# Kernel optimization log

Hardware: AMD Instinct MI355X
Metric: run time of the kernel (lower is better)

## Reference

```python
import jax, jax.numpy as jnp
import numpy as np

N_USER = 50000
N_ITEM = 50000
E = 600000
IN_F = 128
HID = 256
OUT = 256
HEADS = 4
D = HID // HEADS
EPS = 1e-5


def setup_inputs() -> dict:
    key = jax.random.key(0)
    ks = jax.random.split(key, 32)
    inp = {}
    inp['x_user'] = jax.random.normal(ks[0], (N_USER, IN_F), jnp.float32)
    inp['x_item'] = jax.random.normal(ks[1], (N_ITEM, IN_F), jnp.float32)
    inp['ui_src'] = jax.random.randint(ks[2], (E,), 0, N_USER)
    inp['ui_dst'] = jax.random.randint(ks[3], (E,), 0, N_ITEM)
    inp['iu_src'] = jax.random.randint(ks[4], (E,), 0, N_ITEM)
    inp['iu_dst'] = jax.random.randint(ks[5], (E,), 0, N_USER)
    dims = [IN_F, HID, HID, HID]
    i = 6
    for l in range(4):
        din = dims[l]
        inp['W%d' % (l + 1)] = jax.random.normal(ks[i], (2, din, HID), jnp.float32) * (1.0 / np.sqrt(din)); i += 1
        inp['al%d' % (l + 1)] = jax.random.normal(ks[i], (2, HEADS, D), jnp.float32) * 0.1; i += 1
        inp['ar%d' % (l + 1)] = jax.random.normal(ks[i], (2, HEADS, D), jnp.float32) * 0.1; i += 1
        inp['b%d' % (l + 1)] = jnp.zeros((2, HID), jnp.float32); i += 1
    inp['bn_g'] = jnp.ones((3, 2, HID), jnp.float32)
    inp['bn_b'] = jnp.zeros((3, 2, HID), jnp.float32)
    return inp


def gat_conv(x_src, x_dst, src, dst, W, al, ar, b, n_dst):
    # DGL GATConv: shared fc, per-head additive attention, segment softmax over dst.
    H, Dh = al.shape
    z_src = (x_src @ W).reshape(-1, H, Dh)   # [Ns,H,D]
    z_dst = (x_dst @ W).reshape(-1, H, Dh)   # [Nd,H,D]
    el = jnp.sum(z_src * al, axis=-1)        # [Ns,H]
    er = jnp.sum(z_dst * ar, axis=-1)        # [Nd,H]
    e = jax.nn.leaky_relu(el[src] + er[dst], 0.2)          # [E,H]
    m = jax.ops.segment_max(e, dst, num_segments=n_dst)    # [Nd,H]
    ex = jnp.exp(e - m[dst])
    s = jax.ops.segment_sum(ex, dst, num_segments=n_dst)
    alpha = ex / s[dst]                                    # [E,H]
    out = jax.ops.segment_sum(z_src[src] * alpha[:, :, None], dst, num_segments=n_dst)
    return out.reshape(n_dst, H * Dh) + b


def batchnorm(x, g, beta):
    mu = jnp.mean(x, axis=0)
    var = jnp.mean((x - mu) ** 2, axis=0)
    return (x - mu) * jax.lax.rsqrt(var + EPS) * g + beta


def _forward(x_user, x_item, ui_src, ui_dst, iu_src, iu_dst,
             W1, al1, ar1, b1, W2, al2, ar2, b2, W3, al3, ar3, b3, W4, al4, ar4, b4,
             bn_g, bn_b):
    def layer(hu, hi, W, al, ar, b):
        h_item = gat_conv(hu, hi, ui_src, ui_dst, W[0], al[0], ar[0], b[0], N_ITEM)
        h_user = gat_conv(hi, hu, iu_src, iu_dst, W[1], al[1], ar[1], b[1], N_USER)
        return h_user, h_item  # mean over single relation per dst type = identity

    hu, hi = layer(x_user, x_item, W1, al1, ar1, b1)
    hu = jax.nn.leaky_relu(batchnorm(hu, bn_g[0, 0], bn_b[0, 0]), 0.01)
    hi = jax.nn.leaky_relu(batchnorm(hi, bn_g[0, 1], bn_b[0, 1]), 0.01)
    hu, hi = layer(hu, hi, W2, al2, ar2, b2)
    hu = jax.nn.leaky_relu(batchnorm(hu, bn_g[1, 0], bn_b[1, 0]), 0.01)
    hi = jax.nn.leaky_relu(batchnorm(hi, bn_g[1, 1], bn_b[1, 1]), 0.01)
    hu, hi = layer(hu, hi, W3, al3, ar3, b3)
    hu = jnp.tanh(batchnorm(hu, bn_g[2, 0], bn_b[2, 0]))
    hi = jnp.tanh(batchnorm(hi, bn_g[2, 1], bn_b[2, 1]))
    hu, hi = layer(hu, hi, W4, al4, ar4, b4)
    return hu.reshape(-1, OUT), hi.reshape(-1, OUT)


def reference(x_user, x_item, ui_src, ui_dst, iu_src, iu_dst,
              W1, al1, ar1, b1, W2, al2, ar2, b2, W3, al3, ar3, b3, W4, al4, ar4, b4,
              bn_g, bn_b):
    return _forward(x_user, x_item, ui_src, ui_dst, iu_src, iu_dst,
                    W1, al1, ar1, b1, W2, al2, ar2, b2, W3, al3, ar3, b3,
                    W4, al4, ar4, b4, bn_g, bn_b)
```

## Files before the change

### kernel.cpp

```cpp
#include <hip/hip_runtime.h>
#include <hip/hip_bf16.h>
#include <type_traits>

#define NN 50000
#define NE 600000
#define HF 256

typedef float f32x4 __attribute__((ext_vector_type(4)));
typedef _Float16 f16x8 __attribute__((ext_vector_type(8)));
typedef _Float16 f16x4 __attribute__((ext_vector_type(4)));

__global__ __launch_bounds__(256) void k_tofp16_2(const float* __restrict__ A,
                                                  const float* __restrict__ B,
                                                  _Float16* __restrict__ OA,
                                                  _Float16* __restrict__ OB, int n4) {
  int i = blockIdx.x * 256 + threadIdx.x;
  const float* X = (i < n4) ? A : B;
  _Float16* Y = (i < n4) ? OA : OB;
  int j = (i < n4) ? i : i - n4;
  if (j < n4) {
    float4 v = reinterpret_cast<const float4*>(X)[j];
    f16x4 o = {(_Float16)v.x, (_Float16)v.y, (_Float16)v.z, (_Float16)v.w};
    reinterpret_cast<f16x4*>(Y)[j] = o;
  }
}

struct TArgs {
  const float* W[8];
  _Float16* dst[8];
  int K[8];
  int cum[9];
};
__global__ __launch_bounds__(256) void k_transpose_all(TArgs t) {
  int idx = blockIdx.x * 256 + threadIdx.x;
#pragma unroll
  for (int s = 0; s < 8; ++s) {
    if (idx >= t.cum[s] && idx < t.cum[s + 1]) {
      int local = idx - t.cum[s];
      int K = t.K[s];
      int k = local >> 8;
      int n = local & 255;
      t.dst[s][(size_t)n * K + k] = (_Float16)t.W[s][local];
    }
  }
}

__global__ __launch_bounds__(256) void k_makeattn2(const float* __restrict__ Wfull,
                                                   const float* __restrict__ ar,
                                                   int K, float* __restrict__ out) {
  int idx = blockIdx.x * 256 + threadIdx.x;
  if (idx >= 2 * K * 4) return;
  int h = idx & 3;
  int k = (idx >> 2) % K;
  int c = idx / (4 * K);
  const float* W = Wfull + (size_t)c * K * 256;
  const float* a = ar + c * 256 + h * 64;
  const float* wrow = W + (size_t)k * 256 + h * 64;
  float s = 0.f;
#pragma unroll 8
  for (int d = 0; d < 64; ++d) s += wrow[d] * a[d];
  out[(size_t)c * K * 4 + k * 4 + h] = s;
}

__global__ __launch_bounds__(256) void k_gemv_er2(const _Float16* __restrict__ Xi,
                                                  const _Float16* __restrict__ Xu,
                                                  const float* __restrict__ war0,
                                                  const float* __restrict__ war1,
                                                  float* __restrict__ ER0, float* __restrict__ ER1,
                                                  int K) {
  int nb = (NN + 3) / 4;
  int rel = blockIdx.x >= nb;
  int bid = rel ? blockIdx.x - nb : blockIdx.x;
  const _Float16* X = rel ? Xu : Xi;
  const float* wa = rel ? war1 : war0;
  float* out = rel ? ER1 : ER0;
  int wid = bid * 4 + (threadIdx.x >> 6);
  if (wid >= NN) return;
  int lane = threadIdx.x & 63;
  float p0 = 0.f, p1 = 0.f, p2 = 0.f, p3 = 0.f;
  int k0 = lane * 4;
  if (k0 < K) {
    f16x4 x = *reinterpret_cast<const f16x4*>(X + (size_t)wid * K + k0);
    float xv[4] = {(float)x.x, (float)x.y, (float)x.z, (float)x.w};
#pragma unroll
    for (int j = 0; j < 4; ++j) {
      float4 wv = *reinterpret_cast<const float4*>(wa + (k0 + j) * 4);
      p0 += xv[j] * wv.x; p1 += xv[j] * wv.y; p2 += xv[j] * wv.z; p3 += xv[j] * wv.w;
    }
  }
#pragma unroll
  for (int off = 32; off > 0; off >>= 1) {
    p0 += __shfl_down(p0, off); p1 += __shfl_down(p1, off);
    p2 += __shfl_down(p2, off); p3 += __shfl_down(p3, off);
  }
  if (lane == 0)
    *reinterpret_cast<float4*>(out + (size_t)wid * 4) = (float4){p0, p1, p2, p3};
}

__global__ __launch_bounds__(256) void k_gemm2(
    const _Float16* __restrict__ A0, const _Float16* __restrict__ A1,
    const _Float16* __restrict__ Wt0, const _Float16* __restrict__ Wt1,
    _Float16* __restrict__ Z0, _Float16* __restrict__ Z1,
    const float* __restrict__ al0, const float* __restrict__ al1,
    float* __restrict__ EL0, float* __restrict__ EL1,
    int M, int K) {
  int mgrid = (M + 63) / 64;
  int side = blockIdx.x >= mgrid;
  int bid = side ? blockIdx.x - mgrid : blockIdx.x;
  const _Float16* A = side ? A1 : A0;
  const _Float16* Wt = side ? Wt1 : Wt0;
  _Float16* Z = side ? Z1 : Z0;
  const float* al = side ? al1 : al0;
  float* EL = side ? EL1 : EL0;

  int wave = threadIdx.x >> 6;
  int lane = threadIdx.x & 63;
  int lr = lane & 15;
  int kg = lane >> 4;
  int row0 = bid * 64;
  int col0 = wave * 64;
  f32x4 acc[4][4];
#pragma unroll
  for (int i = 0; i < 4; ++i)
#pragma unroll
    for (int j = 0; j < 4; ++j) acc[i][j] = (f32x4){0.f, 0.f, 0.f, 0.f};

  for (int k0 = 0; k0 < K; k0 += 32) {
    f16x8 af[4], bfr[4];
#pragma unroll
    for (int mt = 0; mt < 4; ++mt) {
      int r = row0 + mt * 16 + lr;
      if (r >= M) r = M - 1;
      af[mt] = *reinterpret_cast<const f16x8*>(A + (size_t)r * K + k0 + kg * 8);
    }
#pragma unroll
    for (int ct = 0; ct < 4; ++ct) {
      int c = col0 + ct * 16 + lr;
      bfr[ct] = *reinterpret_cast<const f16x8*>(Wt + (size_t)c * K + k0 + kg * 8);
    }
#pragma unroll
    for (int mt = 0; mt < 4; ++mt)
#pragma unroll
      for (int ct = 0; ct < 4; ++ct)
        acc[mt][ct] = __builtin_amdgcn_mfma_f32_16x16x32_f16(af[mt], bfr[ct], acc[mt][ct], 0, 0, 0);
  }
#pragma unroll
  for (int mt = 0; mt < 4; ++mt) {
#pragma unroll
    for (int r = 0; r < 4; ++r) {
      int row = row0 + mt * 16 + kg * 4 + r;
      if (row < M) {
#pragma unroll
        for (int ct = 0; ct < 4; ++ct) {
          int col = col0 + ct * 16 + lr;
          Z[(size_t)row * HF + col] = (_Float16)acc[mt][ct][r];
        }
      }
    }
  }
  float al4[4];
#pragma unroll
  for (int ct = 0; ct < 4; ++ct) al4[ct] = al[wave * 64 + ct * 16 + lr];
#pragma unroll
  for (int mt = 0; mt < 4; ++mt) {
#pragma unroll
    for (int r = 0; r < 4; ++r) {
      float p = acc[mt][0][r] * al4[0] + acc[mt][1][r] * al4[1] +
                acc[mt][2][r] * al4[2] + acc[mt][3][r] * al4[3];
#pragma unroll
      for (int off = 1; off < 16; off <<= 1) p += __shfl_xor(p, off);
      int row = row0 + mt * 16 + kg * 4 + r;
      if (lr == 0 && row < M) EL[(size_t)row * 4 + wave] = p;
    }
  }
}

__global__ __launch_bounds__(256) void k_hist2(const int* __restrict__ d0, const int* __restrict__ d1,
                                               int* __restrict__ c0, int* __restrict__ c1) {
  int t = blockIdx.x * 256 + threadIdx.x;
  if (t < NE) atomicAdd(&c0[d0[t]], 1);
  else if (t < 2 * NE) atomicAdd(&c1[d1[t - NE]], 1);
}

__global__ __launch_bounds__(1024) void k_scan1_2(const int* __restrict__ c0, const int* __restrict__ c1,
                                                  int* __restrict__ rp0, int* __restrict__ rp1,
                                                  int* __restrict__ b0, int* __restrict__ b1, int nscan) {
  __shared__ int tmp[1024];
  int rel = blockIdx.x >= nscan;
  int blk = rel ? blockIdx.x - nscan : blockIdx.x;
  const int* counts = rel ? c1 : c0;
  int* rp = rel ? rp1 : rp0;
  int* bsum = rel ? b1 : b0;
  int i = blk * 1024 + threadIdx.x;
  int v = (i < NN) ? counts[i] : 0;
  tmp[threadIdx.x] = v;
  __syncthreads();
  for (int off = 1; off < 1024; off <<= 1) {
    int t = (threadIdx.x >= off) ? tmp[threadIdx.x - off] : 0;
    __syncthreads();
    tmp[threadIdx.x] += t;
    __syncthreads();
  }
  if (i < NN) rp[i] = tmp[threadIdx.x] - v;
  if (threadIdx.x == 1023) bsum[blk] = tmp[1023];
}

__global__ __launch_bounds__(128) void k_scan2_2(int* __restrict__ b0, int* __restrict__ b1, int nb) {
  int rel = threadIdx.x >> 6;
  int l = threadIdx.x & 63;
  int* bsum = rel ? b1 : b0;
  int orig = (l < nb) ? bsum[l] : 0;
  int v = orig;
#pragma unroll
  for (int off = 1; off < 64; off <<= 1) {
    int t = __shfl_up(v, off);
    if (l >= off) v += t;
  }
  if (l < nb) bsum[l] = v - orig;
}

__global__ __launch_bounds__(1024) void k_scan3_2(int* __restrict__ rp0, int* __restrict__ rp1,
                                                  const int* __restrict__ b0, const int* __restrict__ b1,
                                                  int nscan) {
  int rel = blockIdx.x >= nscan;
  int blk = rel ? blockIdx.x - nscan : blockIdx.x;
  int* rp = rel ? rp1 : rp0;
  const int* bsum = rel ? b1 : b0;
  int i = blk * 1024 + threadIdx.x;
  if (i < NN) rp[i] += bsum[blk];
  if (i == 0) rp[NN] = NE;
}

__global__ __launch_bounds__(256) void k_scatter2(
    const int* __restrict__ s0, const int* __restrict__ d0,
    const int* __restrict__ s1, const int* __restrict__ d1,
    const int* __restrict__ rp0, const int* __restrict__ rp1,
    int* __restrict__ f0, int* __restrict__ f1,
    int* __restrict__ cs0, int* __restrict__ cs1) {
  int t = blockIdx.x * 256 + threadIdx.x;
  if (t < NE) {
    int d = d0[t];
    int pos = rp0[d] + atomicAdd(&f0[d], 1);
    cs0[pos] = s0[t];
  } else if (t < 2 * NE) {
    int e = t - NE;
    int d = d1[e];
    int pos = rp1[d] + atomicAdd(&f1[d], 1);
    cs1[pos] = s1[e];
  }
}

__device__ __forceinline__ float pick_h(float4 v, int h) {
  float r = v.x;
  r = (h == 1) ? v.y : r;
  r = (h == 2) ? v.z : r;
  r = (h == 3) ? v.w : r;
  return r;
}

template <typename OT>
__global__ __launch_bounds__(256) void k_agg2(
    const int* __restrict__ rpA, const int* __restrict__ csA,
    const float* __restrict__ elA, const float* __restrict__ erA,
    const _Float16* __restrict__ ZA, const float* __restrict__ bA, OT* __restrict__ oA,
    const int* __restrict__ rpB, const int* __restrict__ csB,
    const float* __restrict__ elB, const float* __restrict__ erB,
    const _Float16* __restrict__ ZB, const float* __restrict__ bB, OT* __restrict__ oB) {
  __shared__ float exs[4][256];
  __shared__ int ssrc[4][64];
  int nb = (NN + 3) / 4;
  int rel = blockIdx.x >= nb;
  int bid = rel ? blockIdx.x - nb : blockIdx.x;
  const int* rp = rel ? rpB : rpA;
  const int* csrc = rel ? csB : csA;
  const float* el = rel ? elB : elA;
  const float* er = rel ? erB : erA;
  const _Float16* Z = rel ? ZB : ZA;
  const float* bias = rel ? bB : bA;
  OT* out = rel ? oB : oA;

  int wv = threadIdx.x >> 6;
  int wid = bid * 4 + wv;
  if (wid >= NN) return;
  int lane = threadIdx.x & 63;
  int half = lane >> 5, l5 = lane & 31;
  int c0 = l5 * 8;
  int h = l5 >> 3;
  int beg = rp[wid], end = rp[wid + 1];
  int deg = end - beg;

  if (deg == 0) {
    if (half == 0) {
      float4 b0 = *reinterpret_cast<const float4*>(bias + c0);
      float4 b1 = *reinterpret_cast<const float4*>(bias + c0 + 4);
      if constexpr (std::is_same<OT, float>::value) {
        float4* op = reinterpret_cast<float4*>(out + (size_t)wid * HF + c0);
        op[0] = b0; op[1] = b1;
      } else {
        f16x8 o = {(_Float16)b0.x, (_Float16)b0.y, (_Float16)b0.z, (_Float16)b0.w,
                   (_Float16)b1.x, (_Float16)b1.y, (_Float16)b1.z, (_Float16)b1.w};
        *reinterpret_cast<f16x8*>(out + (size_t)wid * HF + c0) = o;
      }
    }
    return;
  }

  if (deg <= 64) {
    int s = 0;
    float4 x = {-1e30f, -1e30f, -1e30f, -1e30f};
    float4 b = *reinterpret_cast<const float4*>(er + (size_t)wid * 4);
    if (lane < deg) {
      s = csrc[beg + lane];
      float4 a = reinterpret_cast<const float4*>(el)[s];
      x.x = a.x + b.x; x.x = x.x >= 0.f ? x.x : 0.2f * x.x;
      x.y = a.y + b.y; x.y = x.y >= 0.f ? x.y : 0.2f * x.y;
      x.z = a.z + b.z; x.z = x.z >= 0.f ? x.z : 0.2f * x.z;
      x.w = a.w + b.w; x.w = x.w >= 0.f ? x.w : 0.2f * x.w;
    }
    float4 m = x;
#pragma unroll
    for (int off = 32; off > 0; off >>= 1) {
      m.x = fmaxf(m.x, __shfl_xor(m.x, off));
      m.y = fmaxf(m.y, __shfl_xor(m.y, off));
      m.z = fmaxf(m.z, __shfl_xor(m.z, off));
      m.w = fmaxf(m.w, __shfl_xor(m.w, off));
    }
    float4 ex = {0.f, 0.f, 0.f, 0.f};
    if (lane < deg) {
      ex.x = __expf(x.x - m.x);
      ex.y = __expf(x.y - m.y);
      ex.z = __expf(x.z - m.z);
      ex.w = __expf(x.w - m.w);
    }
    float4 sm = ex;
#pragma unroll
    for (int off = 32; off > 0; off >>= 1) {
      sm.x += __shfl_xor(sm.x, off);
      sm.y += __shfl_xor(sm.y, off);
      sm.z += __shfl_xor(sm.z, off);
      sm.w += __shfl_xor(sm.w, off);
    }
    float inv = 1.0f / pick_h(sm, h);
    if (lane < deg) {
      *reinterpret_cast<float4*>(&exs[wv][lane * 4]) = ex;
      ssrc[wv][lane] = s;
    }
    float a8[8] = {0.f, 0.f, 0.f, 0.f, 0.f, 0.f, 0.f, 0.f};
    int j = half;
#define AGG_STEP(J)                                                        \
    {                                                                      \
      int sj = ssrc[wv][(J)];                                              \
      float wj = exs[wv][(J) * 4 + h];                                     \
      f16x8 z = *reinterpret_cast<const f16x8*>(Z + (size_t)sj * HF + c0); \
      _Pragma("unroll")                                                    \
      for (int q = 0; q < 8; ++q) a8[q] += wj * (float)z[q];               \
    }
    for (; j + 6 < deg; j += 8) {
      AGG_STEP(j); AGG_STEP(j + 2); AGG_STEP(j + 4); AGG_STEP(j + 6);
    }
    for (; j < deg; j += 2) { AGG_STEP(j); }
#undef AGG_STEP
#pragma unroll
    for (int q = 0; q < 8; ++q) a8[q] += __shfl_xor(a8[q], 32);
    if (half == 0) {
      float4 b0 = *reinterpret_cast<const float4*>(bias + c0);
      float4 b1 = *reinterpret_cast<const float4*>(bias + c0 + 4);
      float r0 = a8[0] * inv + b0.x, r1 = a8[1] * inv + b0.y;
      float r2 = a8[2] * inv + b0.z, r3 = a8[3] * inv + b0.w;
      float r4 = a8[4] * inv + b1.x, r5 = a8[5] * inv + b1.y;
      float r6 = a8[6] * inv + b1.z, r7 = a8[7] * inv + b1.w;
      if constexpr (std::is_same<OT, float>::value) {
        float4* op = reinterpret_cast<float4*>(out + (size_t)wid * HF + c0);
        op[0] = (float4){r0, r1, r2, r3};
        op[1] = (float4){r4, r5, r6, r7};
      } else {
        f16x8 o = {(_Float16)r0, (_Float16)r1, (_Float16)r2, (_Float16)r3,
                   (_Float16)r4, (_Float16)r5, (_Float16)r6, (_Float16)r7};
        *reinterpret_cast<f16x8*>(out + (size_t)wid * HF + c0) = o;
      }
    }
    return;
  }

  {
    int c4 = lane * 4;
    int h4 = lane >> 4;
    float4 b = *reinterpret_cast<const float4*>(er + (size_t)wid * 4);
    float4 m = {-1e30f, -1e30f, -1e30f, -1e30f};
    for (int e = beg; e < end; ++e) {
      int s = csrc[e];
      float4 a = reinterpret_cast<const float4*>(el)[s];
      float4 x;
      x.x = a.x + b.x; x.x = x.x >= 0.f ? x.x : 0.2f * x.x;
      x.y = a.y + b.y; x.y = x.y >= 0.f ? x.y : 0.2f * x.y;
      x.z = a.z + b.z; x.z = x.z >= 0.f ? x.z : 0.2f * x.z;
      x.w = a.w + b.w; x.w = x.w >= 0.f ? x.w : 0.2f * x.w;
      m.x = fmaxf(m.x, x.x); m.y = fmaxf(m.y, x.y);
      m.z = fmaxf(m.z, x.z); m.w = fmaxf(m.w, x.w);
    }
    float4 sm = {0.f, 0.f, 0.f, 0.f};
    float4 acc = {0.f, 0.f, 0.f, 0.f};
    for (int e = beg; e < end; ++e) {
      int s = csrc[e];
      float4 a = reinterpret_cast<const float4*>(el)[s];
      float4 x;
      x.x = a.x + b.x; x.x = x.x >= 0.f ? x.x : 0.2f * x.x;
      x.y = a.y + b.y; x.y = x.y >= 0.f ? x.y : 0.2f * x.y;
      x.z = a.z + b.z; x.z = x.z >= 0.f ? x.z : 0.2f * x.z;
      x.w = a.w + b.w; x.w = x.w >= 0.f ? x.w : 0.2f * x.w;
      float4 exv;
      exv.x = __expf(x.x - m.x); exv.y = __expf(x.y - m.y);
      exv.z = __expf(x.z - m.z); exv.w = __expf(x.w - m.w);
      sm.x += exv.x; sm.y += exv.y; sm.z += exv.z; sm.w += exv.w;
      float w0 = pick_h(exv, h4);
      f16x4 z0 = *reinterpret_cast<const f16x4*>(Z + (size_t)s * HF + c4);
      acc.x += w0 * (float)z0.x;
      acc.y += w0 * (float)z0.y;
      acc.z += w0 * (float)z0.z;
      acc.w += w0 * (float)z0.w;
    }
    float inv = 1.0f / pick_h(sm, h4);
    float4 bv = *reinterpret_cast<const float4*>(bias + c4);
    float r0 = acc.x * inv + bv.x, r1 = acc.y * inv + bv.y;
    float r2 = acc.z * inv + bv.z, r3 = acc.w * inv + bv.w;
    if constexpr (std::is_same<OT, float>::value) {
      *reinterpret_cast<float4*>(out + (size_t)wid * HF + c4) = (float4){r0, r1, r2, r3};
    } else {
      f16x4 o = {(_Float16)r0, (_Float16)r1, (_Float16)r2, (_Float16)r3};
      *reinterpret_cast<f16x4*>(out + (size_t)wid * HF + c4) = o;
    }
  }
}

__global__ __launch_bounds__(256) void k_bn_stats2(const _Float16* __restrict__ XU,
                                                   const _Float16* __restrict__ XI,
                                                   float* __restrict__ su, float* __restrict__ qu,
                                                   float* __restrict__ si, float* __restrict__ qi) {
  int rel = blockIdx.x >> 9;
  int blk = blockIdx.x & 511;
  const _Float16* X = rel ? XI : XU;
  float* sums = rel ? si : su;
  float* sqs = rel ? qi : qu;
  int c = threadIdx.x;
  float s = 0.f, q = 0.f;
  for (int r = blk; r < NN; r += 512) {
    float v = (float)X[(size_t)r * HF + c];
    s += v;
    q += v * v;
  }
  atomicAdd(&sums[c], s);
  atomicAdd(&sqs[c], q);
}

__global__ __launch_bounds__(256) void k_bn_apply2(
    const _Float16* __restrict__ XU, const _Float16* __restrict__ XI,
    const float* __restrict__ su, const float* __restrict__ qu,
    const float* __restrict__ si, const float* __restrict__ qi,
    const float* __restrict__ gU, const float* __restrict__ btU,
    const float* __restrict__ gI, const float* __restrict__ btI,
    _Float16* __restrict__ YU, _Float16* __restrict__ YI, int act) {
  const int nb = NN * HF / 8 / 256;
  int rel = blockIdx.x >= nb;
  int bid = rel ? blockIdx.x - nb : blockIdx.x;
  const _Float16* X = rel ? XI : XU;
  const float* sums = rel ? si : su;
  const float* sqs = rel ? qi : qu;
  const float* g = rel ? gI : gU;
  const float* bt = rel ? btI : btU;
  _Float16* Y = rel ? YI : YU;
  int gid = bid * 256 + threadIdx.x;
  int i0 = gid * 8;
  int c0 = i0 & 255;
  const float invN = 1.0f / NN;
  f16x8 xv = *reinterpret_cast<const f16x8*>(X + i0);
  float4 s0 = *reinterpret_cast<const float4*>(sums + c0);
  float4 s1 = *reinterpret_cast<const float4*>(sums + c0 + 4);
  float4 q0 = *reinterpret_cast<const float4*>(sqs + c0);
  float4 q1 = *reinterpret_cast<const float4*>(sqs + c0 + 4);
  float4 g0 = *reinterpret_cast<const float4*>(g + c0);
  float4 g1 = *reinterpret_cast<const float4*>(g + c0 + 4);
  float4 b0 = *reinterpret_cast<const float4*>(bt + c0);
  float4 b1 = *reinterpret_cast<const float4*>(bt + c0 + 4);
  float sa[8] = {s0.x, s0.y, s0.z, s0.w, s1.x, s1.y, s1.z, s1.w};
  float qa[8] = {q0.x, q0.y, q0.z, q0.w, q1.x, q1.y, q1.z, q1.w};
  float ga[8] = {g0.x, g0.y, g0.z, g0.w, g1.x, g1.y, g1.z, g1.w};
  float ba[8] = {b0.x, b0.y, b0.z, b0.w, b1.x, b1.y, b1.z, b1.w};
  f16x8 o;
#pragma unroll
  for (int j = 0; j < 8; ++j) {
    float mu = sa[j] * invN;
    float var = qa[j] * invN - mu * mu;
    float sc = rsqrtf(var + 1e-5f) * ga[j];
    float v = ((float)xv[j] - mu) * sc + ba[j];
    v = act ? tanhf(v) : (v >= 0.f ? v : 0.01f * v);
    o[j] = (_Float16)v;
  }
  *reinterpret_cast<f16x8*>(Y + i0) = o;
}

extern "C" void kernel_launch(void* const* d_in, const int* in_sizes, int n_in,
                              void* d_out, int out_size, void* d_ws, size_t ws_size,
                              hipStream_t stream) {
  (void)in_sizes; (void)n_in; (void)out_size; (void)ws_size;
  const float* x_user = (const float*)d_in[0];
  const float* x_item = (const float*)d_in[1];
  const int* ui_src = (const int*)d_in[2];
  const int* ui_dst = (const int*)d_in[3];
  const int* iu_src = (const int*)d_in[4];
  const int* iu_dst = (const int*)d_in[5];
  const float *Wp[4], *alp[4], *arp[4], *bp[4];
  for (int l = 0; l < 4; ++l) {
    Wp[l]  = (const float*)d_in[6 + 4 * l];
    alp[l] = (const float*)d_in[7 + 4 * l];
    arp[l] = (const float*)d_in[8 + 4 * l];
    bp[l]  = (const float*)d_in[9 + 4 * l];
  }
  const float* bng = (const float*)d_in[22];
  const float* bnb = (const float*)d_in[23];

  char* w = (char*)d_ws;
  auto alloc = [&](size_t bytes) -> void* {
    void* p = (void*)w;
    w += (bytes + 255) & ~(size_t)255;
    return p;
  };
  _Float16* XU16 = (_Float16*)alloc((size_t)NN * 128 * 2);
  _Float16* XI16 = (_Float16*)alloc((size_t)NN * 128 * 2);
  _Float16* H16U = (_Float16*)alloc((size_t)NN * HF * 2);
  _Float16* H16I = (_Float16*)alloc((size_t)NN * HF * 2);
  _Float16* Z0 = (_Float16*)alloc((size_t)NN * HF * 2);
  _Float16* Z1 = (_Float16*)alloc((size_t)NN * HF * 2);
  _Float16* RAW16U = (_Float16*)alloc((size_t)NN * HF * 2);
  _Float16* RAW16I = (_Float16*)alloc((size_t)NN * HF * 2);
  float* EL0 = (float*)alloc((size_t)NN * 4 * 4);
  float* ER0 = (float*)alloc((size_t)NN * 4 * 4);
  float* EL1 = (float*)alloc((size_t)NN * 4 * 4);
  float* ER1 = (float*)alloc((size_t)NN * 4 * 4);
  _Float16* WT = (_Float16*)alloc((size_t)8 * 65536 * 2);
  float* ATTN = (float*)alloc((size_t)2 * 256 * 4 * 4);
  int* rp_ui = (int*)alloc((size_t)(NN + 1) * 4);
  int* rp_iu = (int*)alloc((size_t)(NN + 1) * 4);
  int* csrc_ui = (int*)alloc((size_t)NE * 4);
  int* csrc_iu = (int*)alloc((size_t)NE * 4);
  int* counts = (int*)alloc((size_t)4 * NN * 4);
  int* bsum_ui = (int*)alloc((size_t)64 * 4);
  int* bsum_iu = (int*)alloc((size_t)64 * 4);
  float* stats = (float*)alloc((size_t)6 * 512 * 4);

  int* counts_ui = counts;
  int* counts_iu = counts + NN;
  int* fill_ui = counts + 2 * NN;
  int* fill_iu = counts + 3 * NN;

  hipMemsetAsync(counts, 0, (size_t)4 * NN * 4, stream);
  hipMemsetAsync(stats, 0, (size_t)6 * 512 * 4, stream);

  int n4 = NN * 128 / 4;
  k_tofp16_2<<<(2 * n4 + 255) / 256, 256, 0, stream>>>(x_user, x_item, XU16, XI16, n4);

  TArgs ta;
  int cum = 0;
  for (int l = 0; l < 4; ++l) {
    int K = (l == 0) ? 128 : 256;
    for (int r = 0; r < 2; ++r) {
      int s = l * 2 + r;
      ta.W[s] = Wp[l] + (size_t)r * K * HF;
      ta.dst[s] = WT + (size_t)s * 65536;
      ta.K[s] = K;
      ta.cum[s] = cum;
      cum += K * 256;
    }
  }
  ta.cum[8] = cum;
  k_transpose_all<<<(cum + 255) / 256, 256, 0, stream>>>(ta);

  int egrid2 = (2 * NE + 255) / 256;
  int nscan = (NN + 1023) / 1024;
  k_hist2<<<egrid2, 256, 0, stream>>>(ui_dst, iu_dst, counts_ui, counts_iu);
  k_scan1_2<<<2 * nscan, 1024, 0, stream>>>(counts_ui, counts_iu, rp_ui, rp_iu, bsum_ui, bsum_iu, nscan);
  k_scan2_2<<<1, 128, 0, stream>>>(bsum_ui, bsum_iu, nscan);
  k_scan3_2<<<2 * nscan, 1024, 0, stream>>>(rp_ui, rp_iu, bsum_ui, bsum_iu, nscan);
  k_scatter2<<<egrid2, 256, 0, stream>>>(ui_src, ui_dst, iu_src, iu_dst, rp_ui, rp_iu,
                                         fill_ui, fill_iu, csrc_ui, csrc_iu);

  const _Float16* hu16 = XU16;
  const _Float16* hi16 = XI16;
  int agrid = (NN + 3) / 4;
  float* out_user = (float*)d_out;
  float* out_item = (float*)d_out + (size_t)NN * HF;

  for (int l = 0; l < 4; ++l) {
    int K = (l == 0) ? 128 : 256;
    const _Float16* W0t = WT + (size_t)(l * 2 + 0) * 65536;
    const _Float16* W1t = WT + (size_t)(l * 2 + 1) * 65536;
    int mgrid = (NN + 63) / 64;

    k_makeattn2<<<(2 * K * 4 + 255) / 256, 256, 0, stream>>>(Wp[l], arp[l], K, ATTN);
    k_gemv_er2<<<2 * agrid, 256, 0, stream>>>(hi16, hu16, ATTN, ATTN + (size_t)K * 4, ER0, ER1, K);

    k_gemm2<<<2 * mgrid, 256, 0, stream>>>(hu16, hi16, W0t, W1t, Z0, Z1,
                                           alp[l] + 0, alp[l] + 256, EL0, EL1, NN, K);

    if (l < 3)
      k_agg2<_Float16><<<2 * agrid, 256, 0, stream>>>(
          rp_ui, csrc_ui, EL0, ER0, Z0, bp[l] + 0, RAW16I,
          rp_iu, csrc_iu, EL1, ER1, Z1, bp[l] + 256, RAW16U);
    else
      k_agg2<float><<<2 * agrid, 256, 0, stream>>>(
          rp_ui, csrc_ui, EL0, ER0, Z0, bp[l] + 0, out_item,
          rp_iu, csrc_iu, EL1, ER1, Z1, bp[l] + 256, out_user);

    if (l < 3) {
      int act = (l == 2) ? 1 : 0;
      float* su = stats + (size_t)(l * 2 + 0) * 512;
      float* qu = su + 256;
      float* si = stats + (size_t)(l * 2 + 1) * 512;
      float* qi = si + 256;
      k_bn_stats2<<<1024, 256, 0, stream>>>(RAW16U, RAW16I, su, qu, si, qi);
      k_bn_apply2<<<2 * (NN * HF / 8 / 256), 256, 0, stream>>>(
          RAW16U, RAW16I, su, qu, si, qi,
          bng + (size_t)(l * 2 + 0) * 256, bnb + (size_t)(l * 2 + 0) * 256,
          bng + (size_t)(l * 2 + 1) * 256, bnb + (size_t)(l * 2 + 1) * 256,
          H16U, H16I, act);
      hu16 = H16U;
      hi16 = H16I;
    }
  }
}
```

Baseline: 1.125 ms.

## Fuse batchnorm-apply and ER gemv into GEMM prologue/epilogue; precompute attention vectors once

Removes the separate batchnorm-apply kernel by applying scale/shift and activation to A tiles as they are loaded in the GEMM. Also folds the ER gemv into the same GEMM kernel: each block recomputes the destination-side attention projection for its 64 rows. The attention-weight vectors for all layers are computed once up front instead of per layer. This saves writing and re-reading the normalized activations and several launches, at the cost of redundant BN parameter math and extra ALU in the GEMM inner loop.

```diff
diff --git a/kernel.cpp b/kernel.cpp
--- a/kernel.cpp
+++ b/kernel.cpp
@@ -45,73 +45,92 @@
   }
 }
 
-__global__ __launch_bounds__(256) void k_makeattn2(const float* __restrict__ Wfull,
-                                                   const float* __restrict__ ar,
-                                                   int K, float* __restrict__ out) {
+__global__ __launch_bounds__(256) void k_makeattn_all(
+    const float* __restrict__ W1, const float* __restrict__ W2,
+    const float* __restrict__ W3, const float* __restrict__ W4,
+    const float* __restrict__ ar1, const float* __restrict__ ar2,
+    const float* __restrict__ ar3, const float* __restrict__ ar4,
+    float* __restrict__ out) {
   int idx = blockIdx.x * 256 + threadIdx.x;
-  if (idx >= 2 * K * 4) return;
+  if (idx >= 8 * 256 * 4) return;
   int h = idx & 3;
-  int k = (idx >> 2) % K;
-  int c = idx / (4 * K);
-  const float* W = Wfull + (size_t)c * K * 256;
-  const float* a = ar + c * 256 + h * 64;
+  int k = (idx >> 2) & 255;
+  int s = idx >> 10;
+  int l = s >> 1, r = s & 1;
+  int K = (l == 0) ? 128 : 256;
+  if (k >= K) return;
+  const float* W = (l == 0 ? W1 : l == 1 ? W2 : l == 2 ? W3 : W4) + (size_t)r * K * 256;
+  const float* a = (l == 0 ? ar1 : l == 1 ? ar2 : l == 2 ? ar3 : ar4) + r * 256 + h * 64;
   const float* wrow = W + (size_t)k * 256 + h * 64;
-  float s = 0.f;
+  float sum = 0.f;
 #pragma unroll 8
-  for (int d = 0; d < 64; ++d) s += wrow[d] * a[d];
-  out[(size_t)c * K * 4 + k * 4 + h] = s;
-}
-
-__global__ __launch_bounds__(256) void k_gemv_er2(const _Float16* __restrict__ Xi,
-                                                  const _Float16* __restrict__ Xu,
-                                                  const float* __restrict__ war0,
-                                                  const float* __restrict__ war1,
-                                                  float* __restrict__ ER0, float* __restrict__ ER1,
-                                                  int K) {
-  int nb = (NN + 3) / 4;
-  int rel = blockIdx.x >= nb;
-  int bid = rel ? blockIdx.x - nb : blockIdx.x;
-  const _Float16* X = rel ? Xu : Xi;
-  const float* wa = rel ? war1 : war0;
-  float* out = rel ? ER1 : ER0;
-  int wid = bid * 4 + (threadIdx.x >> 6);
-  if (wid >= NN) return;
-  int lane = threadIdx.x & 63;
-  float p0 = 0.f, p1 = 0.f, p2 = 0.f, p3 = 0.f;
-  int k0 = lane * 4;
-  if (k0 < K) {
-    f16x4 x = *reinterpret_cast<const f16x4*>(X + (size_t)wid * K + k0);
-    float xv[4] = {(float)x.x, (float)x.y, (float)x.z, (float)x.w};
-#pragma unroll
-    for (int j = 0; j < 4; ++j) {
-      float4 wv = *reinterpret_cast<const float4*>(wa + (k0 + j) * 4);
-      p0 += xv[j] * wv.x; p1 += xv[j] * wv.y; p2 += xv[j] * wv.z; p3 += xv[j] * wv.w;
-    }
-  }
-#pragma unroll
-  for (int off = 32; off > 0; off >>= 1) {
-    p0 += __shfl_down(p0, off); p1 += __shfl_down(p1, off);
-    p2 += __shfl_down(p2, off); p3 += __shfl_down(p3, off);
-  }
-  if (lane == 0)
-    *reinterpret_cast<float4*>(out + (size_t)wid * 4) = (float4){p0, p1, p2, p3};
-}
-
-__global__ __launch_bounds__(256) void k_gemm2(
-    const _Float16* __restrict__ A0, const _Float16* __restrict__ A1,
-    const _Float16* __restrict__ Wt0, const _Float16* __restrict__ Wt1,
-    _Float16* __restrict__ Z0, _Float16* __restrict__ Z1,
-    const float* __restrict__ al0, const float* __restrict__ al1,
-    float* __restrict__ EL0, float* __restrict__ EL1,
-    int M, int K) {
-  int mgrid = (M + 63) / 64;
+  for (int d = 0; d < 64; ++d) sum += wrow[d] * a[d];
+  out[s * 1024 + k * 4 + h] = sum;
+}
+
+__device__ __forceinline__ void bnparams8(const float* __restrict__ sums,
+                                          const float* __restrict__ sqs,
+                                          const float* __restrict__ g,
+                                          const float* __restrict__ bt,
+                                          int k, float* scale, float* shift) {
+  const float invN = 1.0f / NN;
+  float4 s0 = *reinterpret_cast<const float4*>(sums + k);
+  float4 s1 = *reinterpret_cast<const float4*>(sums + k + 4);
+  float4 q0 = *reinterpret_cast<const float4*>(sqs + k);
+  float4 q1 = *reinterpret_cast<const float4*>(sqs + k + 4);
+  float4 g0 = *reinterpret_cast<const float4*>(g + k);
+  float4 g1 = *reinterpret_cast<const float4*>(g + k + 4);
+  float4 b0 = *reinterpret_cast<const float4*>(bt + k);
+  float4 b1 = *reinterpret_cast<const float4*>(bt + k + 4);
+  float sa[8] = {s0.x, s0.y, s0.z, s0.w, s1.x, s1.y, s1.z, s1.w};
+  float qa[8] = {q0.x, q0.y, q0.z, q0.w, q1.x, q1.y, q1.z, q1.w};
+  float ga[8] = {g0.x, g0.y, g0.z, g0.w, g1.x, g1.y, g1.z, g1.w};
+  float ba[8] = {b0.x, b0.y, b0.z, b0.w, b1.x, b1.y, b1.z, b1.w};
+#pragma unroll
+  for (int j = 0; j < 8; ++j) {
+    float mu = sa[j] * invN;
+    float var = qa[j] * invN - mu * mu;
+    float rs = rsqrtf(var + 1e-5f) * ga[j];
+    scale[j] = rs;
+    shift[j] = ba[j] - mu * rs;
+  }
+}
+
+__device__ __forceinline__ float actf(float v, int mode) {
+  if (mode == 1) return v >= 0.f ? v : 0.01f * v;
+  if (mode == 2) return tanhf(v);
+  return v;
+}
+
+struct GArgs {
+  const _Float16* A0; const _Float16* A1;
+  const _Float16* Wt0; const _Float16* Wt1;
+  _Float16* Z0; _Float16* Z1;
+  const float* al0; const float* al1;
+  float* EL0; float* EL1;
+  const float* war_s0; const float* war_s1;
+  float* ER_s0; float* ER_s1;
+  const float* su; const float* qu; const float* gu; const float* bu;
+  const float* si; const float* qi; const float* gi; const float* bi;
+  int M, K, mode;
+};
+
+__global__ __launch_bounds__(256) void k_gemm3(GArgs ga) {
+  int mgrid = (ga.M + 63) / 64;
   int side = blockIdx.x >= mgrid;
   int bid = side ? blockIdx.x - mgrid : blockIdx.x;
-  const _Float16* A = side ? A1 : A0;
-  const _Float16* Wt = side ? Wt1 : Wt0;
-  _Float16* Z = side ? Z1 : Z0;
-  const float* al = side ? al1 : al0;
-  float* EL = side ? EL1 : EL0;
+  const _Float16* A = side ? ga.A1 : ga.A0;
+  const _Float16* Wt = side ? ga.Wt1 : ga.Wt0;
+  _Float16* Z = side ? ga.Z1 : ga.Z0;
+  const float* al = side ? ga.al1 : ga.al0;
+  float* EL = side ? ga.EL1 : ga.EL0;
+  const float* war = side ? ga.war_s1 : ga.war_s0;
+  float* ER = side ? ga.ER_s1 : ga.ER_s0;
+  const float* sums = side ? ga.si : ga.su;
+  const float* sqs = side ? ga.qi : ga.qu;
+  const float* gg = side ? ga.gi : ga.gu;
+  const float* bb = side ? ga.bi : ga.bu;
+  const int K = ga.K, M = ga.M, mode = ga.mode;
 
   int wave = threadIdx.x >> 6;
   int lane = threadIdx.x & 63;
@@ -126,12 +145,25 @@
     for (int j = 0; j < 4; ++j) acc[i][j] = (f32x4){0.f, 0.f, 0.f, 0.f};
 
   for (int k0 = 0; k0 < K; k0 += 32) {
+    float scale[8], shift[8];
+    if (mode) bnparams8(sums, sqs, gg, bb, k0 + kg * 8, scale, shift);
     f16x8 af[4], bfr[4];
 #pragma unroll
     for (int mt = 0; mt < 4; ++mt) {
       int r = row0 + mt * 16 + lr;
       if (r >= M) r = M - 1;
-      af[mt] = *reinterpret_cast<const f16x8*>(A + (size_t)r * K + k0 + kg * 8);
+      f16x8 raw = *reinterpret_cast<const f16x8*>(A + (size_t)r * K + k0 + kg * 8);
+      if (mode) {
+        f16x8 o;
+#pragma unroll
+        for (int j = 0; j < 8; ++j) {
+          float v = (float)raw[j] * scale[j] + shift[j];
+          o[j] = (_Float16)actf(v, mode);
+        }
+        af[mt] = o;
+      } else {
+        af[mt] = raw;
+      }
     }
 #pragma unroll
     for (int ct = 0; ct < 4; ++ct) {
@@ -172,6 +204,38 @@
       int row = row0 + mt * 16 + kg * 4 + r;
       if (lr == 0 && row < M) EL[(size_t)row * 4 + wave] = p;
     }
+  }
+  {
+    int rl = threadIdx.x >> 2;
+    int q = threadIdx.x & 3;
+    int row = row0 + rl;
+    int rowc = row < M ? row : M - 1;
+    int kq = q * (K >> 2);
+    float p0 = 0.f, p1 = 0.f, p2 = 0.f, p3 = 0.f;
+    for (int k = kq; k < kq + (K >> 2); k += 8) {
+      f16x8 raw = *reinterpret_cast<const f16x8*>(A + (size_t)rowc * K + k);
+      float va[8];
+      if (mode) {
+        float scale[8], shift[8];
+        bnparams8(sums, sqs, gg, bb, k, scale, shift);
+#pragma unroll
+        for (int j = 0; j < 8; ++j) va[j] = actf((float)raw[j] * scale[j] + shift[j], mode);
+      } else {
+#pragma unroll
+        for (int j = 0; j < 8; ++j) va[j] = (float)raw[j];
+      }
+#pragma unroll
+      for (int j = 0; j < 8; ++j) {
+        float4 wv = *reinterpret_cast<const float4*>(war + (k + j) * 4);
+        p0 += va[j] * wv.x; p1 += va[j] * wv.y; p2 += va[j] * wv.z; p3 += va[j] * wv.w;
+      }
+    }
+    p0 += __shfl_xor(p0, 1); p0 += __shfl_xor(p0, 2);
+    p1 += __shfl_xor(p1, 1); p1 += __shfl_xor(p1, 2);
+    p2 += __shfl_xor(p2, 1); p2 += __shfl_xor(p2, 2);
+    p3 += __shfl_xor(p3, 1); p3 += __shfl_xor(p3, 2);
+    if (q == 0 && row < M)
+      *reinterpret_cast<float4*>(ER + (size_t)row * 4) = (float4){p0, p1, p2, p3};
   }
 }
 
@@ -452,52 +516,6 @@
   atomicAdd(&sqs[c], q);
 }
 
-__global__ __launch_bounds__(256) void k_bn_apply2(
-    const _Float16* __restrict__ XU, const _Float16* __restrict__ XI,
-    const float* __restrict__ su, const float* __restrict__ qu,
-    const float* __restrict__ si, const float* __restrict__ qi,
-    const float* __restrict__ gU, const float* __restrict__ btU,
-    const float* __restrict__ gI, const float* __restrict__ btI,
-    _Float16* __restrict__ YU, _Float16* __restrict__ YI, int act) {
-  const int nb = NN * HF / 8 / 256;
-  int rel = blockIdx.x >= nb;
-  int bid = rel ? blockIdx.x - nb : blockIdx.x;
-  const _Float16* X = rel ? XI : XU;
-  const float* sums = rel ? si : su;
-  const float* sqs = rel ? qi : qu;
-  const float* g = rel ? gI : gU;
-  const float* bt = rel ? btI : btU;
-  _Float16* Y = rel ? YI : YU;
-  int gid = bid * 256 + threadIdx.x;
-  int i0 = gid * 8;
-  int c0 = i0 & 255;
-  const float invN = 1.0f / NN;
-  f16x8 xv = *reinterpret_cast<const f16x8*>(X + i0);
-  float4 s0 = *reinterpret_cast<const float4*>(sums + c0);
-  float4 s1 = *reinterpret_cast<const float4*>(sums + c0 + 4);
-  float4 q0 = *reinterpret_cast<const float4*>(sqs + c0);
-  float4 q1 = *reinterpret_cast<const float4*>(sqs + c0 + 4);
-  float4 g0 = *reinterpret_cast<const float4*>(g + c0);
-  float4 g1 = *reinterpret_cast<const float4*>(g + c0 + 4);
-  float4 b0 = *reinterpret_cast<const float4*>(bt + c0);
-  float4 b1 = *reinterpret_cast<const float4*>(bt + c0 + 4);
-  float sa[8] = {s0.x, s0.y, s0.z, s0.w, s1.x, s1.y, s1.z, s1.w};
-  float qa[8] = {q0.x, q0.y, q0.z, q0.w, q1.x, q1.y, q1.z, q1.w};
-  float ga[8] = {g0.x, g0.y, g0.z, g0.w, g1.x, g1.y, g1.z, g1.w};
-  float ba[8] = {b0.x, b0.y, b0.z, b0.w, b1.x, b1.y, b1.z, b1.w};
-  f16x8 o;
-#pragma unroll
-  for (int j = 0; j < 8; ++j) {
-    float mu = sa[j] * invN;
-    float var = qa[j] * invN - mu * mu;
-    float sc = rsqrtf(var + 1e-5f) * ga[j];
-    float v = ((float)xv[j] - mu) * sc + ba[j];
-    v = act ? tanhf(v) : (v >= 0.f ? v : 0.01f * v);
-    o[j] = (_Float16)v;
-  }
-  *reinterpret_cast<f16x8*>(Y + i0) = o;
-}
-
 extern "C" void kernel_launch(void* const* d_in, const int* in_sizes, int n_in,
                               void* d_out, int out_size, void* d_ws, size_t ws_size,
                               hipStream_t stream) {
@@ -526,8 +544,6 @@
   };
   _Float16* XU16 = (_Float16*)alloc((size_t)NN * 128 * 2);
   _Float16* XI16 = (_Float16*)alloc((size_t)NN * 128 * 2);
-  _Float16* H16U = (_Float16*)alloc((size_t)NN * HF * 2);
-  _Float16* H16I = (_Float16*)alloc((size_t)NN * HF * 2);
   _Float16* Z0 = (_Float16*)alloc((size_t)NN * HF * 2);
   _Float16* Z1 = (_Float16*)alloc((size_t)NN * HF * 2);
   _Float16* RAW16U = (_Float16*)alloc((size_t)NN * HF * 2);
@@ -537,7 +553,7 @@
   float* EL1 = (float*)alloc((size_t)NN * 4 * 4);
   float* ER1 = (float*)alloc((size_t)NN * 4 * 4);
   _Float16* WT = (_Float16*)alloc((size_t)8 * 65536 * 2);
-  float* ATTN = (float*)alloc((size_t)2 * 256 * 4 * 4);
+  float* ATTN = (float*)alloc((size_t)8 * 1024 * 4);
   int* rp_ui = (int*)alloc((size_t)(NN + 1) * 4);
   int* rp_iu = (int*)alloc((size_t)(NN + 1) * 4);
   int* csrc_ui = (int*)alloc((size_t)NE * 4);
@@ -574,6 +590,9 @@
   ta.cum[8] = cum;
   k_transpose_all<<<(cum + 255) / 256, 256, 0, stream>>>(ta);
 
+  k_makeattn_all<<<(8 * 256 * 4 + 255) / 256, 256, 0, stream>>>(
+      Wp[0], Wp[1], Wp[2], Wp[3], arp[0], arp[1], arp[2], arp[3], ATTN);
+
   int egrid2 = (2 * NE + 255) / 256;
   int nscan = (NN + 1023) / 1024;
   k_hist2<<<egrid2, 256, 0, stream>>>(ui_dst, iu_dst, counts_ui, counts_iu);
@@ -583,23 +602,41 @@
   k_scatter2<<<egrid2, 256, 0, stream>>>(ui_src, ui_dst, iu_src, iu_dst, rp_ui, rp_iu,
                                          fill_ui, fill_iu, csrc_ui, csrc_iu);
 
-  const _Float16* hu16 = XU16;
-  const _Float16* hi16 = XI16;
   int agrid = (NN + 3) / 4;
   float* out_user = (float*)d_out;
   float* out_item = (float*)d_out + (size_t)NN * HF;
 
   for (int l = 0; l < 4; ++l) {
     int K = (l == 0) ? 128 : 256;
-    const _Float16* W0t = WT + (size_t)(l * 2 + 0) * 65536;
-    const _Float16* W1t = WT + (size_t)(l * 2 + 1) * 65536;
     int mgrid = (NN + 63) / 64;
 
-    k_makeattn2<<<(2 * K * 4 + 255) / 256, 256, 0, stream>>>(Wp[l], arp[l], K, ATTN);
-    k_gemv_er2<<<2 * agrid, 256, 0, stream>>>(hi16, hu16, ATTN, ATTN + (size_t)K * 4, ER0, ER1, K);
-
-    k_gemm2<<<2 * mgrid, 256, 0, stream>>>(hu16, hi16, W0t, W1t, Z0, Z1,
-                                           alp[l] + 0, alp[l] + 256, EL0, EL1, NN, K);
+    GArgs ga;
+    ga.A0 = (l == 0) ? XU16 : RAW16U;
+    ga.A1 = (l == 0) ? XI16 : RAW16I;
+    ga.Wt0 = WT + (size_t)(l * 2 + 0) * 65536;
+    ga.Wt1 = WT + (size_t)(l * 2 + 1) * 65536;
+    ga.Z0 = Z0; ga.Z1 = Z1;
+    ga.al0 = alp[l] + 0; ga.al1 = alp[l] + 256;
+    ga.EL0 = EL0; ga.EL1 = EL1;
+    ga.war_s0 = ATTN + (size_t)(l * 2 + 1) * 1024;
+    ga.war_s1 = ATTN + (size_t)(l * 2 + 0) * 1024;
+    ga.ER_s0 = ER1; ga.ER_s1 = ER0;
+    if (l > 0) {
+      const float* su = stats + (size_t)((l - 1) * 2 + 0) * 512;
+      const float* si = stats + (size_t)((l - 1) * 2 + 1) * 512;
+      ga.su = su; ga.qu = su + 256;
+      ga.si = si; ga.qi = si + 256;
+      ga.gu = bng + (size_t)((l - 1) * 2 + 0) * 256;
+      ga.bu = bnb + (size_t)((l - 1) * 2 + 0) * 256;
+      ga.gi = bng + (size_t)((l - 1) * 2 + 1) * 256;
+      ga.bi = bnb + (size_t)((l - 1) * 2 + 1) * 256;
+      ga.mode = (l == 3) ? 2 : 1;
+    } else {
+      ga.su = ga.qu = ga.si = ga.qi = ga.gu = ga.bu = ga.gi = ga.bi = nullptr;
+      ga.mode = 0;
+    }
+    ga.M = NN; ga.K = K;
+    k_gemm3<<<2 * mgrid, 256, 0, stream>>>(ga);
 
     if (l < 3)
       k_agg2<_Float16><<<2 * agrid, 256, 0, stream>>>(
@@ -611,19 +648,11 @@
           rp_iu, csrc_iu, EL1, ER1, Z1, bp[l] + 256, out_user);
 
     if (l < 3) {
-      int act = (l == 2) ? 1 : 0;
       float* su = stats + (size_t)(l * 2 + 0) * 512;
       float* qu = su + 256;
       float* si = stats + (size_t)(l * 2 + 1) * 512;
       float* qi = si + 256;
       k_bn_stats2<<<1024, 256, 0, stream>>>(RAW16U, RAW16I, su, qu, si, qi);
-      k_bn_apply2<<<2 * (NN * HF / 8 / 256), 256, 0, stream>>>(
-          RAW16U, RAW16I, su, qu, si, qi,
-          bng + (size_t)(l * 2 + 0) * 256, bnb + (size_t)(l * 2 + 0) * 256,
-          bng + (size_t)(l * 2 + 1) * 256, bnb + (size_t)(l * 2 + 1) * 256,
-          H16U, H16I, act);
-      hu16 = H16U;
-      hi16 = H16I;
-    }
-  }
-}
+    }
+  }
+}
```

New measurement: 1.449 ms. 28.7% more time.

## Stage GEMM A tiles through double-buffered swizzled LDS and precompute all attention vectors

Applied to the files above, without the earlier changes.

The feature GEMM now loads A tiles into a double-buffered LDS array with an XOR swizzle, using direct global-to-LDS loads, so the next K-slab is prefetched while the current one feeds the MFMAs. Weight fragments are still read straight from global memory. The per-layer attention projection kernels are merged into one launch before the layer loop, which removes three launches. The cost is an extra barrier per K-slab and LDS use that may limit occupancy.

```diff
diff --git a/kernel.cpp b/kernel.cpp
--- a/kernel.cpp
+++ b/kernel.cpp
@@ -45,21 +45,27 @@
   }
 }
 
-__global__ __launch_bounds__(256) void k_makeattn2(const float* __restrict__ Wfull,
-                                                   const float* __restrict__ ar,
-                                                   int K, float* __restrict__ out) {
+__global__ __launch_bounds__(256) void k_makeattn_all(
+    const float* __restrict__ W1, const float* __restrict__ W2,
+    const float* __restrict__ W3, const float* __restrict__ W4,
+    const float* __restrict__ ar1, const float* __restrict__ ar2,
+    const float* __restrict__ ar3, const float* __restrict__ ar4,
+    float* __restrict__ out) {
   int idx = blockIdx.x * 256 + threadIdx.x;
-  if (idx >= 2 * K * 4) return;
+  if (idx >= 8 * 256 * 4) return;
   int h = idx & 3;
-  int k = (idx >> 2) % K;
-  int c = idx / (4 * K);
-  const float* W = Wfull + (size_t)c * K * 256;
-  const float* a = ar + c * 256 + h * 64;
+  int k = (idx >> 2) & 255;
+  int s = idx >> 10;
+  int l = s >> 1, r = s & 1;
+  int K = (l == 0) ? 128 : 256;
+  if (k >= K) return;
+  const float* W = (l == 0 ? W1 : l == 1 ? W2 : l == 2 ? W3 : W4) + (size_t)r * K * 256;
+  const float* a = (l == 0 ? ar1 : l == 1 ? ar2 : l == 2 ? ar3 : ar4) + r * 256 + h * 64;
   const float* wrow = W + (size_t)k * 256 + h * 64;
-  float s = 0.f;
+  float sum = 0.f;
 #pragma unroll 8
-  for (int d = 0; d < 64; ++d) s += wrow[d] * a[d];
-  out[(size_t)c * K * 4 + k * 4 + h] = s;
+  for (int d = 0; d < 64; ++d) sum += wrow[d] * a[d];
+  out[s * 1024 + k * 4 + h] = sum;
 }
 
 __global__ __launch_bounds__(256) void k_gemv_er2(const _Float16* __restrict__ Xi,
@@ -97,53 +103,84 @@
     *reinterpret_cast<float4*>(out + (size_t)wid * 4) = (float4){p0, p1, p2, p3};
 }
 
-__global__ __launch_bounds__(256) void k_gemm2(
-    const _Float16* __restrict__ A0, const _Float16* __restrict__ A1,
-    const _Float16* __restrict__ Wt0, const _Float16* __restrict__ Wt1,
-    _Float16* __restrict__ Z0, _Float16* __restrict__ Z1,
-    const float* __restrict__ al0, const float* __restrict__ al1,
-    float* __restrict__ EL0, float* __restrict__ EL1,
-    int M, int K) {
-  int mgrid = (M + 63) / 64;
-  int side = blockIdx.x >= mgrid;
-  int bid = side ? blockIdx.x - mgrid : blockIdx.x;
-  const _Float16* A = side ? A1 : A0;
-  const _Float16* Wt = side ? Wt1 : Wt0;
-  _Float16* Z = side ? Z1 : Z0;
-  const float* al = side ? al1 : al0;
-  float* EL = side ? EL1 : EL0;
-
+struct GArgs {
+  const _Float16* A0; const _Float16* A1;
+  const _Float16* Wt0; const _Float16* Wt1;
+  _Float16* Z0; _Float16* Z1;
+  const float* al0; const float* al1;
+  float* EL0; float* EL1;
+  int M, K;
+};
+
+__global__ __launch_bounds__(256) void k_gemm5(GArgs ga) {
+  __shared__ _Float16 As[2][64 * 64];
+  const int nrow = (NN + 63) / 64;
+  int side = blockIdx.x >= nrow;
+  int bid = side ? blockIdx.x - nrow : blockIdx.x;
+  const _Float16* A = side ? ga.A1 : ga.A0;
+  const _Float16* Wt = side ? ga.Wt1 : ga.Wt0;
+  _Float16* Z = side ? ga.Z1 : ga.Z0;
+  const float* al = side ? ga.al1 : ga.al0;
+  float* EL = side ? ga.EL1 : ga.EL0;
+  const int K = ga.K, M = ga.M;
+  int row0 = bid * 64;
   int wave = threadIdx.x >> 6;
   int lane = threadIdx.x & 63;
-  int lr = lane & 15;
-  int kg = lane >> 4;
-  int row0 = bid * 64;
+  int lr = lane & 15, kg = lane >> 4;
   int col0 = wave * 64;
+
+  auto stage = [&](int buf, int k0) {
+#pragma unroll
+    for (int j = 0; j < 2; ++j) {
+      int Lb = j * 4096 + wave * 1024;
+      int L = Lb + lane * 16;
+      int r = L >> 7;
+      int kb = (L & 127) ^ ((r & 7) << 4);
+      int rg = row0 + r; rg = rg < M ? rg : M - 1;
+      const char* gsrc = (const char*)A + ((size_t)rg * K + k0) * 2 + kb;
+      char* ldst = (char*)(&As[buf][0]) + Lb;
+      __builtin_amdgcn_global_load_lds(
+          (const __attribute__((address_space(1))) unsigned int*)gsrc,
+          (__attribute__((address_space(3))) unsigned int*)ldst, 16, 0, 0);
+    }
+  };
+
   f32x4 acc[4][4];
 #pragma unroll
   for (int i = 0; i < 4; ++i)
 #pragma unroll
     for (int j = 0; j < 4; ++j) acc[i][j] = (f32x4){0.f, 0.f, 0.f, 0.f};
 
-  for (int k0 = 0; k0 < K; k0 += 32) {
-    f16x8 af[4], bfr[4];
-#pragma unroll
-    for (int mt = 0; mt < 4; ++mt) {
-      int r = row0 + mt * 16 + lr;
-      if (r >= M) r = M - 1;
-      af[mt] = *reinterpret_cast<const f16x8*>(A + (size_t)r * K + k0 + kg * 8);
-    }
-#pragma unroll
-    for (int ct = 0; ct < 4; ++ct) {
-      int c = col0 + ct * 16 + lr;
-      bfr[ct] = *reinterpret_cast<const f16x8*>(Wt + (size_t)c * K + k0 + kg * 8);
-    }
-#pragma unroll
-    for (int mt = 0; mt < 4; ++mt)
-#pragma unroll
-      for (int ct = 0; ct < 4; ++ct)
-        acc[mt][ct] = __builtin_amdgcn_mfma_f32_16x16x32_f16(af[mt], bfr[ct], acc[mt][ct], 0, 0, 0);
-  }
+  int nt = K >> 6;
+  stage(0, 0);
+  __syncthreads();
+  for (int t = 0; t < nt; ++t) {
+    if (t + 1 < nt) stage((t + 1) & 1, (t + 1) * 64);
+    const char* abuf = (const char*)(&As[t & 1][0]);
+#pragma unroll
+    for (int s = 0; s < 2; ++s) {
+      int kk = t * 64 + s * 32 + kg * 8;
+      f16x8 af[4], bfr[4];
+#pragma unroll
+      for (int mt = 0; mt < 4; ++mt) {
+        int r = mt * 16 + lr;
+        int cb = ((s << 6) | (kg << 4)) ^ ((r & 7) << 4);
+        af[mt] = *reinterpret_cast<const f16x8*>(abuf + r * 128 + cb);
+      }
+#pragma unroll
+      for (int ct = 0; ct < 4; ++ct) {
+        int c = col0 + ct * 16 + lr;
+        bfr[ct] = *reinterpret_cast<const f16x8*>(Wt + (size_t)c * K + kk);
+      }
+#pragma unroll
+      for (int mt = 0; mt < 4; ++mt)
+#pragma unroll
+        for (int ct = 0; ct < 4; ++ct)
+          acc[mt][ct] = __builtin_amdgcn_mfma_f32_16x16x32_f16(af[mt], bfr[ct], acc[mt][ct], 0, 0, 0);
+    }
+    __syncthreads();
+  }
+
 #pragma unroll
   for (int mt = 0; mt < 4; ++mt) {
 #pragma unroll
@@ -160,7 +197,7 @@
   }
   float al4[4];
 #pragma unroll
-  for (int ct = 0; ct < 4; ++ct) al4[ct] = al[wave * 64 + ct * 16 + lr];
+  for (int ct = 0; ct < 4; ++ct) al4[ct] = al[col0 + ct * 16 + lr];
 #pragma unroll
   for (int mt = 0; mt < 4; ++mt) {
 #pragma unroll
@@ -537,7 +574,7 @@
   float* EL1 = (float*)alloc((size_t)NN * 4 * 4);
   float* ER1 = (float*)alloc((size_t)NN * 4 * 4);
   _Float16* WT = (_Float16*)alloc((size_t)8 * 65536 * 2);
-  float* ATTN = (float*)alloc((size_t)2 * 256 * 4 * 4);
+  float* ATTN = (float*)alloc((size_t)8 * 1024 * 4);
   int* rp_ui = (int*)alloc((size_t)(NN + 1) * 4);
   int* rp_iu = (int*)alloc((size_t)(NN + 1) * 4);
   int* csrc_ui = (int*)alloc((size_t)NE * 4);
@@ -574,6 +611,9 @@
   ta.cum[8] = cum;
   k_transpose_all<<<(cum + 255) / 256, 256, 0, stream>>>(ta);
 
+  k_makeattn_all<<<(8 * 256 * 4 + 255) / 256, 256, 0, stream>>>(
+      Wp[0], Wp[1], Wp[2], Wp[3], arp[0], arp[1], arp[2], arp[3], ATTN);
+
   int egrid2 = (2 * NE + 255) / 256;
   int nscan = (NN + 1023) / 1024;
   k_hist2<<<egrid2, 256, 0, stream>>>(ui_dst, iu_dst, counts_ui, counts_iu);
@@ -583,23 +623,29 @@
   k_scatter2<<<egrid2, 256, 0, stream>>>(ui_src, ui_dst, iu_src, iu_dst, rp_ui, rp_iu,
                                          fill_ui, fill_iu, csrc_ui, csrc_iu);
 
-  const _Float16* hu16 = XU16;
-  const _Float16* hi16 = XI16;
   int agrid = (NN + 3) / 4;
+  int nrow = (NN + 63) / 64;
   float* out_user = (float*)d_out;
   float* out_item = (float*)d_out + (size_t)NN * HF;
 
   for (int l = 0; l < 4; ++l) {
     int K = (l == 0) ? 128 : 256;
-    const _Float16* W0t = WT + (size_t)(l * 2 + 0) * 65536;
-    const _Float16* W1t = WT + (size_t)(l * 2 + 1) * 65536;
-    int mgrid = (NN + 63) / 64;
-
-    k_makeattn2<<<(2 * K * 4 + 255) / 256, 256, 0, stream>>>(Wp[l], arp[l], K, ATTN);
-    k_gemv_er2<<<2 * agrid, 256, 0, stream>>>(hi16, hu16, ATTN, ATTN + (size_t)K * 4, ER0, ER1, K);
-
-    k_gemm2<<<2 * mgrid, 256, 0, stream>>>(hu16, hi16, W0t, W1t, Z0, Z1,
-                                           alp[l] + 0, alp[l] + 256, EL0, EL1, NN, K);
+    const _Float16* Au = (l == 0) ? XU16 : H16U;
+    const _Float16* Ai = (l == 0) ? XI16 : H16I;
+    const float* war0 = ATTN + (size_t)(l * 2 + 0) * 1024;
+    const float* war1 = ATTN + (size_t)(l * 2 + 1) * 1024;
+
+    k_gemv_er2<<<2 * agrid, 256, 0, stream>>>(Ai, Au, war0, war1, ER0, ER1, K);
+
+    GArgs ga;
+    ga.A0 = Au; ga.A1 = Ai;
+    ga.Wt0 = WT + (size_t)(l * 2 + 0) * 65536;
+    ga.Wt1 = WT + (size_t)(l * 2 + 1) * 65536;
+    ga.Z0 = Z0; ga.Z1 = Z1;
+    ga.al0 = alp[l] + 0; ga.al1 = alp[l] + 256;
+    ga.EL0 = EL0; ga.EL1 = EL1;
+    ga.M = NN; ga.K = K;
+    k_gemm5<<<2 * nrow, 256, 0, stream>>>(ga);
 
     if (l < 3)
       k_agg2<_Float16><<<2 * agrid, 256, 0, stream>>>(
@@ -613,17 +659,13 @@
     if (l < 3) {
       int act = (l == 2) ? 1 : 0;
       float* su = stats + (size_t)(l * 2 + 0) * 512;
-      float* qu = su + 256;
       float* si = stats + (size_t)(l * 2 + 1) * 512;
-      float* qi = si + 256;
-      k_bn_stats2<<<1024, 256, 0, stream>>>(RAW16U, RAW16I, su, qu, si, qi);
+      k_bn_stats2<<<1024, 256, 0, stream>>>(RAW16U, RAW16I, su, su + 256, si, si + 256);
       k_bn_apply2<<<2 * (NN * HF / 8 / 256), 256, 0, stream>>>(
-          RAW16U, RAW16I, su, qu, si, qi,
+          RAW16U, RAW16I, su, su + 256, si, si + 256,
           bng + (size_t)(l * 2 + 0) * 256, bnb + (size_t)(l * 2 + 0) * 256,
           bng + (size_t)(l * 2 + 1) * 256, bnb + (size_t)(l * 2 + 1) * 256,
           H16U, H16I, act);
-      hu16 = H16U;
-      hi16 = H16I;
-    }
-  }
-}
+    }
+  }
+}
```

After: 1.048 ms. 1.07x faster.
